# Performance work log

Measured on AMD Instinct MI355X. Metric: run time of the kernel, lower is better.

The kernel has to match this reference:

```python
import jax, jax.numpy as jnp
import numpy as np

D_OUT = 10          # number of classes (d_out)
TEMP = 1.0          # temperature T
EPS = 1e-07         # log eps from original code


def setup_inputs() -> dict:
    key = jax.random.key(0)
    k1, k2, k3, k4, k5 = jax.random.split(key, 5)
    N, M, d_in, dim = 2048, 131072, 128, 128
    x = jax.random.normal(k1, (N, d_in), dtype=jnp.float32)
    candidate_x = jax.random.normal(k2, (M, d_in), dtype=jnp.float32)
    candidate_y = jax.random.randint(k3, (M,), 0, D_OUT)
    # encoder = nn.Linear(d_in, dim): weight [dim, d_in], bias [dim]
    W = jax.random.normal(k4, (dim, d_in), dtype=jnp.float32) / np.float32(np.sqrt(d_in))
    b = jax.random.normal(k5, (dim,), dtype=jnp.float32) * 0.01
    return {"x": x, "candidate_x": candidate_x, "candidate_y": candidate_y, "W": W, "b": b}


def reference(x, candidate_x, candidate_y, W, b):
    # encoder (mode=0, n_blocks=0): single linear layer
    z = x @ W.T + b                 # [N, dim]
    zc = candidate_x @ W.T + b      # [M, dim]
    # torch.cdist(z, zc, p=2): pairwise euclidean distances [N, M]
    sq = (jnp.sum(z * z, axis=-1, keepdims=True)
          + jnp.sum(zc * zc, axis=-1)[None, :]
          - 2.0 * (z @ zc.T))
    dist = jnp.sqrt(jnp.maximum(sq, 1e-12)) / TEMP
    # is_train=False: no diagonal masking, no candidate subsampling
    probs = jax.nn.softmax(-dist, axis=-1)            # [N, M]
    onehot = jax.nn.one_hot(candidate_y, D_OUT, dtype=z.dtype)  # [M, D_OUT]
    logits = probs @ onehot                           # [N, D_OUT]
    return jnp.log(logits + EPS)
```

## Files before the change

kernel.cpp:

```cpp
#include <hip/hip_runtime.h>
#include <stdint.h>
#include <math.h>

#define N_ROWS 2048
#define M_CAND 131072
#define DIMK 128
#define DOUT 10
#define COLS_PER_BLOCK 1024
#define SUB_ITERS 16
#define CHUNKS_MAX 138
#define M_PAD_MAX (CHUNKS_MAX * COLS_PER_BLOCK)
#define LOG2E 1.4426950408889634f
#define L2E2 (LOG2E * LOG2E)

typedef __attribute__((ext_vector_type(8))) __bf16 bf16x8;
typedef __attribute__((ext_vector_type(8))) short s16x8;
typedef __attribute__((ext_vector_type(4))) float f32x4;
typedef __attribute__((address_space(3))) void lds_void;
typedef const __attribute__((address_space(1))) void gbl_void;

__device__ __forceinline__ short f2bf(float f) {
  union { float f; unsigned u; } v; v.f = f;
  return (short)((v.u + 0x7fffu + ((v.u >> 16) & 1u)) >> 16);
}
__device__ __forceinline__ float bf2f(short h) {
  union { unsigned u; float f; } v;
  v.u = ((unsigned)(unsigned short)h) << 16; return v.f;
}
__device__ __forceinline__ float fast_sqrtf(float x) {
#if __has_builtin(__builtin_amdgcn_sqrtf)
  return __builtin_amdgcn_sqrtf(x);
#else
  return sqrtf(x);
#endif
}
__device__ __forceinline__ float fast_exp2f(float x) {
#if __has_builtin(__builtin_amdgcn_exp2f)
  return __builtin_amdgcn_exp2f(x);
#else
  return exp2f(x);
#endif
}

__device__ __forceinline__ void stage64(const short* gbase, short* lds, int t) {
  int w = t >> 6;
#pragma unroll
  for (int i = 0; i < 4; ++i) {
    int flat = i * 256 + t;
    int r = flat >> 4, s = flat & 15;
    int g = s ^ (r & 15);
    const short* src = gbase + r * DIMK + g * 8;
    short* dst = lds + (i * 256 + w * 64) * 8;
    __builtin_amdgcn_global_load_lds((gbl_void*)src, (lds_void*)dst, 16, 0, 0);
  }
}

__device__ __forceinline__ void stage128(const short* gbase, short* lds, int t) {
  int w = t >> 6;
#pragma unroll
  for (int i = 0; i < 8; ++i) {
    int flat = i * 256 + t;
    int r = flat >> 4, s = flat & 15;
    int g = s ^ (r & 15);
    const short* src = gbase + r * DIMK + g * 8;
    short* dst = lds + (i * 256 + w * 64) * 8;
    __builtin_amdgcn_global_load_lds((gbl_void*)src, (lds_void*)dst, 16, 0, 0);
  }
}

__device__ __forceinline__ void mfma_tile(const short* As, const short* Bs,
                                          f32x4 acc[4][4], int wrow, int wcol,
                                          int quad, int l15) {
#pragma unroll
  for (int ks = 0; ks < 4; ++ks) {
    int slot = (ks * 4 + quad) ^ l15;
    bf16x8 a[4], b[4];
#pragma unroll
    for (int i = 0; i < 4; ++i) {
      a[i] = *(const bf16x8*)(As + (wrow + i * 16 + l15) * DIMK + slot * 8);
      b[i] = *(const bf16x8*)(Bs + (wcol + i * 16 + l15) * DIMK + slot * 8);
    }
#pragma unroll
    for (int i = 0; i < 4; ++i)
#pragma unroll
      for (int j = 0; j < 4; ++j)
        acc[i][j] = __builtin_amdgcn_mfma_f32_16x16x32_bf16(a[i], b[j], acc[i][j], 0, 0, 0);
  }
}

__global__ __launch_bounds__(256) void fill_kernel(int* __restrict__ p, int v, int n) {
  int i = blockIdx.x * 256 + threadIdx.x;
  if (i < n) p[i] = v;
}

__global__ __launch_bounds__(256) void hist_kernel(const int* __restrict__ y,
                                                   int* __restrict__ cnt) {
  __shared__ int h[DOUT];
  int t = threadIdx.x;
  if (t < DOUT) h[t] = 0;
  __syncthreads();
  atomicAdd(&h[y[blockIdx.x * 256 + t]], 1);
  __syncthreads();
  if (t < DOUT) cnt[blockIdx.x * DOUT + t] = h[t];
}

__global__ __launch_bounds__(512) void scan_kernel(const int* __restrict__ cnt,
                                                   int* __restrict__ blockoff,
                                                   int* __restrict__ chunk_class) {
  __shared__ int buf[2][512 * DOUT];
  __shared__ int pbnd[DOUT + 1];
  int t = threadIdx.x;
  int v[DOUT];
#pragma unroll
  for (int c = 0; c < DOUT; ++c) { v[c] = cnt[t * DOUT + c]; buf[0][t * DOUT + c] = v[c]; }
  __syncthreads();
  int src = 0;
  for (int off = 1; off < 512; off <<= 1) {
    int x[DOUT];
#pragma unroll
    for (int c = 0; c < DOUT; ++c) {
      x[c] = buf[src][t * DOUT + c];
      if (t >= off) x[c] += buf[src][(t - off) * DOUT + c];
    }
#pragma unroll
    for (int c = 0; c < DOUT; ++c) buf[1 - src][t * DOUT + c] = x[c];
    src ^= 1;
    __syncthreads();
  }
  if (t == 0) {
    int pb = 0;
    pbnd[0] = 0;
    for (int c = 0; c < DOUT; ++c) {
      int tot = buf[src][511 * DOUT + c];
      pb += (tot + COLS_PER_BLOCK - 1) & ~(COLS_PER_BLOCK - 1);
      pbnd[c + 1] = pb;
    }
  }
  __syncthreads();
  if (t < CHUNKS_MAX) {
    int col = t * COLS_PER_BLOCK, c = 0;
#pragma unroll
    for (int k = 1; k < DOUT; ++k) c += (col >= pbnd[k]) ? 1 : 0;
    chunk_class[t] = c;
  }
#pragma unroll
  for (int c = 0; c < DOUT; ++c)
    blockoff[t * DOUT + c] = pbnd[c] + buf[src][t * DOUT + c] - v[c];
}

__global__ __launch_bounds__(256) void scatter_kernel(const int* __restrict__ y,
                                                      const int* __restrict__ blockoff,
                                                      int* __restrict__ invperm) {
  __shared__ int cur[DOUT];
  int t = threadIdx.x;
  if (t < DOUT) cur[t] = blockoff[blockIdx.x * DOUT + t];
  __syncthreads();
  int e = blockIdx.x * 256 + t;
  int p = atomicAdd(&cur[y[e]], 1);
  invperm[p] = e;
}

__global__ __launch_bounds__(256, 2) void encoder_kernel(
    const float* __restrict__ X, const float* __restrict__ W,
    const float* __restrict__ bias, const int* __restrict__ invperm,
    short* __restrict__ Zb, float* __restrict__ Sq) {
  __shared__ __align__(16) short As[DIMK * DIMK];
  __shared__ __align__(16) short Bs[DIMK * DIMK];
  __shared__ float bias_s[DIMK];
  __shared__ float sqacc[DIMK];
  int t = threadIdx.x;
  int rowbase = blockIdx.x * 128;
  if (t < DIMK) { bias_s[t] = bias[t]; sqacc[t] = 0.f; }
#pragma unroll
  for (int i = 0; i < 8; ++i) {
    int flat = i * 256 + t;
    int r = flat >> 4, sl = flat & 15;
    int g = sl ^ (r & 15);
    const float* srcW = W + r * DIMK + g * 8;
    float4 a0 = *(const float4*)srcW;
    float4 a1 = *(const float4*)(srcW + 4);
    s16x8 wv;
    wv[0] = f2bf(a0.x); wv[1] = f2bf(a0.y); wv[2] = f2bf(a0.z); wv[3] = f2bf(a0.w);
    wv[4] = f2bf(a1.x); wv[5] = f2bf(a1.y); wv[6] = f2bf(a1.z); wv[7] = f2bf(a1.w);
    *(s16x8*)(Bs + r * DIMK + sl * 8) = wv;
    int xr = rowbase + r;
    int gxr = invperm ? invperm[xr] : xr;
    const float* srcX = X + (size_t)(gxr < 0 ? 0 : gxr) * DIMK + g * 8;
    float4 b0 = *(const float4*)srcX;
    float4 b1 = *(const float4*)(srcX + 4);
    if (gxr < 0) { b0 = make_float4(0.f, 0.f, 0.f, 0.f); b1 = b0; }
    s16x8 xv;
    xv[0] = f2bf(b0.x); xv[1] = f2bf(b0.y); xv[2] = f2bf(b0.z); xv[3] = f2bf(b0.w);
    xv[4] = f2bf(b1.x); xv[5] = f2bf(b1.y); xv[6] = f2bf(b1.z); xv[7] = f2bf(b1.w);
    *(s16x8*)(As + r * DIMK + sl * 8) = xv;
  }
  __syncthreads();
  int lane = t & 63, wid = t >> 6;
  int quad = lane >> 4, l15 = lane & 15;
  int wrow = (wid >> 1) * 64, wcol = (wid & 1) * 64;
  f32x4 acc[4][4];
  f32x4 z4 = {0.f, 0.f, 0.f, 0.f};
#pragma unroll
  for (int i = 0; i < 4; ++i)
#pragma unroll
    for (int j = 0; j < 4; ++j) acc[i][j] = z4;
  mfma_tile(As, Bs, acc, wrow, wcol, quad, l15);
#pragma unroll
  for (int ti = 0; ti < 4; ++ti) {
#pragma unroll
    for (int r = 0; r < 4; ++r) {
      int row_l = wrow + ti * 16 + quad * 4 + r;
      size_t grow = (size_t)(rowbase + row_l);
      float sqp = 0.f;
#pragma unroll
      for (int j = 0; j < 4; ++j) {
        int dcol = wcol + j * 16 + l15;
        float z = acc[ti][j][r] + bias_s[dcol];
        short hb = f2bf(z);
        float zr = bf2f(hb);
        sqp += zr * zr;
        Zb[grow * DIMK + dcol] = hb;
      }
      sqp += __shfl_xor(sqp, 1);
      sqp += __shfl_xor(sqp, 2);
      sqp += __shfl_xor(sqp, 4);
      sqp += __shfl_xor(sqp, 8);
      if (l15 == 0) atomicAdd(&sqacc[row_l], sqp);
    }
  }
  __syncthreads();
  if (t < DIMK) {
    bool dead = invperm && (invperm[rowbase + t] < 0);
    Sq[rowbase + t] = dead ? 1e30f : sqacc[t];
  }
}

__global__ __launch_bounds__(256, 4) void nca_main(
    const short* __restrict__ Zb, const short* __restrict__ Cb,
    const float* __restrict__ Sqz, const float* __restrict__ Sqc,
    float* __restrict__ partials) {
  __shared__ __align__(16) short Bs[2][64 * DIMK];
  __shared__ float sqc_s[COLS_PER_BLOCK];

  int t = threadIdx.x;
  int lane = t & 63, wid = t >> 6;
  int quad = lane >> 4, l15 = lane & 15;
  int wrow = wid * 32;
  int rowbase = blockIdx.x * 128;
  int colbase0 = blockIdx.y * COLS_PER_BLOCK;

  stage64(Cb + (size_t)colbase0 * DIMK, &Bs[0][0], t);

#pragma unroll
  for (int i = 0; i < 4; ++i)
    sqc_s[i * 256 + t] = Sqc[colbase0 + i * 256 + t] * L2E2;

  bf16x8 afrag[4][2];
#pragma unroll
  for (int ks = 0; ks < 4; ++ks)
#pragma unroll
    for (int ti = 0; ti < 2; ++ti)
      afrag[ks][ti] = *(const bf16x8*)(
          Zb + (size_t)(rowbase + wrow + ti * 16 + l15) * DIMK + ks * 32 + quad * 8);

  float szv[2][4];
#pragma unroll
  for (int ti = 0; ti < 2; ++ti)
#pragma unroll
    for (int r = 0; r < 4; ++r)
      szv[ti][r] = Sqz[rowbase + wrow + ti * 16 + quad * 4 + r] * L2E2;

  float sum[8];
#pragma unroll
  for (int i = 0; i < 8; ++i) sum[i] = 0.f;

  for (int it = 0; it < SUB_ITERS; ++it) {
    __syncthreads();
    if (it + 1 < SUB_ITERS)
      stage64(Cb + (size_t)(colbase0 + (it + 1) * 64) * DIMK, &Bs[(it + 1) & 1][0], t);
    const short* B = &Bs[it & 1][0];

    f32x4 acc[2][4];
    f32x4 z4 = {0.f, 0.f, 0.f, 0.f};
#pragma unroll
    for (int ti = 0; ti < 2; ++ti)
#pragma unroll
      for (int j = 0; j < 4; ++j) acc[ti][j] = z4;

#pragma unroll
    for (int ks = 0; ks < 4; ++ks) {
      int slot = (ks * 4 + quad) ^ l15;
      bf16x8 b[4];
#pragma unroll
      for (int j = 0; j < 4; ++j)
        b[j] = *(const bf16x8*)(B + (j * 16 + l15) * DIMK + slot * 8);
#pragma unroll
      for (int ti = 0; ti < 2; ++ti)
#pragma unroll
        for (int j = 0; j < 4; ++j)
          acc[ti][j] = __builtin_amdgcn_mfma_f32_16x16x32_bf16(afrag[ks][ti], b[j],
                                                               acc[ti][j], 0, 0, 0);
    }

    float sqcv[4];
#pragma unroll
    for (int j = 0; j < 4; ++j) sqcv[j] = sqc_s[it * 64 + j * 16 + l15];
#pragma unroll
    for (int ti = 0; ti < 2; ++ti)
#pragma unroll
      for (int r = 0; r < 4; ++r) {
        float base = szv[ti][r];
        float v[4];
#pragma unroll
        for (int j = 0; j < 4; ++j) {
          float sq = fmaf(acc[ti][j][r], -2.0f * L2E2, base + sqcv[j]);
          float d = fast_sqrtf(__builtin_fabsf(sq));
          v[j] = fast_exp2f(-d);
        }
        sum[ti * 4 + r] += (v[0] + v[1]) + (v[2] + v[3]);
      }
  }

#pragma unroll
  for (int si = 0; si < 8; ++si) {
    float s = sum[si];
    s += __shfl_xor(s, 1);
    s += __shfl_xor(s, 2);
    s += __shfl_xor(s, 4);
    s += __shfl_xor(s, 8);
    if (l15 == 0) {
      int row_l = wrow + (si >> 2) * 16 + quad * 4 + (si & 3);
      partials[(size_t)blockIdx.y * N_ROWS + rowbase + row_l] = s;
    }
  }
}

__global__ __launch_bounds__(64) void reduce_kernel(const float* __restrict__ partials,
                                                    const int* __restrict__ chunk_class,
                                                    float* __restrict__ out) {
  int row = blockIdx.x, lane = threadIdx.x;
  float s = 0.f;
  for (int ch = 0; ch < CHUNKS_MAX; ++ch) {
    float p = partials[(size_t)ch * N_ROWS + row];
    int c = chunk_class[ch];
    s += (lane == c) ? p : 0.f;
  }
  float tot = s;
  tot += __shfl_xor(tot, 1);
  tot += __shfl_xor(tot, 2);
  tot += __shfl_xor(tot, 4);
  tot += __shfl_xor(tot, 8);
  tot += __shfl_xor(tot, 16);
  tot += __shfl_xor(tot, 32);
  if (lane < DOUT)
    out[(size_t)row * DOUT + lane] = logf(s / tot + 1e-7f);
}

extern "C" void kernel_launch(void* const* d_in, const int* in_sizes, int n_in,
                              void* d_out, int out_size, void* d_ws, size_t ws_size,
                              hipStream_t stream) {
  const float* x = (const float*)d_in[0];
  const float* cx = (const float*)d_in[1];
  const int* cy = (const int*)d_in[2];
  const float* W = (const float*)d_in[3];
  const float* bias = (const float*)d_in[4];
  float* out = (float*)d_out;
  char* ws = (char*)d_ws;

  size_t off = 0;
  auto alloc = [&](size_t bytes) {
    void* p = ws + off;
    off = (off + bytes + 255) & ~(size_t)255;
    return p;
  };
  short* Zb = (short*)alloc((size_t)N_ROWS * DIMK * 2);
  short* Cb = (short*)alloc((size_t)M_PAD_MAX * DIMK * 2);
  float* Sqz = (float*)alloc((size_t)N_ROWS * 4);
  float* Sqc = (float*)alloc((size_t)M_PAD_MAX * 4);
  int* invperm = (int*)alloc((size_t)M_PAD_MAX * 4);
  int* cnt = (int*)alloc(512 * DOUT * 4);
  int* blockoff = (int*)alloc(512 * DOUT * 4);
  int* chunk_class = (int*)alloc(CHUNKS_MAX * 4);
  float* partials = (float*)alloc((size_t)CHUNKS_MAX * N_ROWS * 4);
  if (off > ws_size) return;

  fill_kernel<<<(M_PAD_MAX + 255) / 256, 256, 0, stream>>>(invperm, -1, M_PAD_MAX);
  hist_kernel<<<M_CAND / 256, 256, 0, stream>>>(cy, cnt);
  scan_kernel<<<1, 512, 0, stream>>>(cnt, blockoff, chunk_class);
  scatter_kernel<<<M_CAND / 256, 256, 0, stream>>>(cy, blockoff, invperm);
  encoder_kernel<<<N_ROWS / 128, 256, 0, stream>>>(x, W, bias, nullptr, Zb, Sqz);
  encoder_kernel<<<M_PAD_MAX / 128, 256, 0, stream>>>(cx, W, bias, invperm, Cb, Sqc);
  nca_main<<<dim3(N_ROWS / 128, CHUNKS_MAX), 256, 0, stream>>>(Zb, Cb, Sqz, Sqc, partials);
  reduce_kernel<<<N_ROWS, 64, 0, stream>>>(partials, chunk_class, out);
}
```

Before: 262.9 us.

## Remove per-class chunk padding; split mixed-class chunks with masked sums and atomics

```diff
diff --git a/kernel.cpp b/kernel.cpp
--- a/kernel.cpp
+++ b/kernel.cpp
@@ -8,14 +8,14 @@
 #define DOUT 10
 #define COLS_PER_BLOCK 1024
 #define SUB_ITERS 16
-#define CHUNKS_MAX 138
-#define M_PAD_MAX (CHUNKS_MAX * COLS_PER_BLOCK)
+#define CHUNKS (M_CAND / COLS_PER_BLOCK)
 #define LOG2E 1.4426950408889634f
 #define L2E2 (LOG2E * LOG2E)
 
 typedef __attribute__((ext_vector_type(8))) __bf16 bf16x8;
 typedef __attribute__((ext_vector_type(8))) short s16x8;
 typedef __attribute__((ext_vector_type(4))) float f32x4;
+typedef __attribute__((ext_vector_type(2))) float f32x2;
 typedef __attribute__((address_space(3))) void lds_void;
 typedef const __attribute__((address_space(1))) void gbl_void;
 
@@ -55,19 +55,6 @@
   }
 }
 
-__device__ __forceinline__ void stage128(const short* gbase, short* lds, int t) {
-  int w = t >> 6;
-#pragma unroll
-  for (int i = 0; i < 8; ++i) {
-    int flat = i * 256 + t;
-    int r = flat >> 4, s = flat & 15;
-    int g = s ^ (r & 15);
-    const short* src = gbase + r * DIMK + g * 8;
-    short* dst = lds + (i * 256 + w * 64) * 8;
-    __builtin_amdgcn_global_load_lds((gbl_void*)src, (lds_void*)dst, 16, 0, 0);
-  }
-}
-
 __device__ __forceinline__ void mfma_tile(const short* As, const short* Bs,
                                           f32x4 acc[4][4], int wrow, int wcol,
                                           int quad, int l15) {
@@ -88,15 +75,12 @@
   }
 }
 
-__global__ __launch_bounds__(256) void fill_kernel(int* __restrict__ p, int v, int n) {
-  int i = blockIdx.x * 256 + threadIdx.x;
-  if (i < n) p[i] = v;
-}
-
 __global__ __launch_bounds__(256) void hist_kernel(const int* __restrict__ y,
-                                                   int* __restrict__ cnt) {
+                                                   int* __restrict__ cnt,
+                                                   float* __restrict__ accum) {
   __shared__ int h[DOUT];
   int t = threadIdx.x;
+  if (blockIdx.x < 128) accum[blockIdx.x * 256 + t] = 0.f;
   if (t < DOUT) h[t] = 0;
   __syncthreads();
   atomicAdd(&h[y[blockIdx.x * 256 + t]], 1);
@@ -106,9 +90,9 @@
 
 __global__ __launch_bounds__(512) void scan_kernel(const int* __restrict__ cnt,
                                                    int* __restrict__ blockoff,
-                                                   int* __restrict__ chunk_class) {
+                                                   int* __restrict__ bnd_g) {
   __shared__ int buf[2][512 * DOUT];
-  __shared__ int pbnd[DOUT + 1];
+  __shared__ int bnd[DOUT + 1];
   int t = threadIdx.x;
   int v[DOUT];
 #pragma unroll
@@ -128,24 +112,14 @@
     __syncthreads();
   }
   if (t == 0) {
-    int pb = 0;
-    pbnd[0] = 0;
-    for (int c = 0; c < DOUT; ++c) {
-      int tot = buf[src][511 * DOUT + c];
-      pb += (tot + COLS_PER_BLOCK - 1) & ~(COLS_PER_BLOCK - 1);
-      pbnd[c + 1] = pb;
-    }
-  }
-  __syncthreads();
-  if (t < CHUNKS_MAX) {
-    int col = t * COLS_PER_BLOCK, c = 0;
-#pragma unroll
-    for (int k = 1; k < DOUT; ++k) c += (col >= pbnd[k]) ? 1 : 0;
-    chunk_class[t] = c;
-  }
+    bnd[0] = 0;
+    for (int c = 0; c < DOUT; ++c) bnd[c + 1] = bnd[c] + buf[src][511 * DOUT + c];
+    for (int k = 0; k <= DOUT; ++k) bnd_g[k] = bnd[k];
+  }
+  __syncthreads();
 #pragma unroll
   for (int c = 0; c < DOUT; ++c)
-    blockoff[t * DOUT + c] = pbnd[c] + buf[src][t * DOUT + c] - v[c];
+    blockoff[t * DOUT + c] = bnd[c] + buf[src][t * DOUT + c] - v[c];
 }
 
 __global__ __launch_bounds__(256) void scatter_kernel(const int* __restrict__ y,
@@ -185,10 +159,9 @@
     *(s16x8*)(Bs + r * DIMK + sl * 8) = wv;
     int xr = rowbase + r;
     int gxr = invperm ? invperm[xr] : xr;
-    const float* srcX = X + (size_t)(gxr < 0 ? 0 : gxr) * DIMK + g * 8;
+    const float* srcX = X + (size_t)gxr * DIMK + g * 8;
     float4 b0 = *(const float4*)srcX;
     float4 b1 = *(const float4*)(srcX + 4);
-    if (gxr < 0) { b0 = make_float4(0.f, 0.f, 0.f, 0.f); b1 = b0; }
     s16x8 xv;
     xv[0] = f2bf(b0.x); xv[1] = f2bf(b0.y); xv[2] = f2bf(b0.z); xv[3] = f2bf(b0.w);
     xv[4] = f2bf(b1.x); xv[5] = f2bf(b1.y); xv[6] = f2bf(b1.z); xv[7] = f2bf(b1.w);
@@ -229,18 +202,14 @@
     }
   }
   __syncthreads();
-  if (t < DIMK) {
-    bool dead = invperm && (invperm[rowbase + t] < 0);
-    Sq[rowbase + t] = dead ? 1e30f : sqacc[t];
-  }
-}
-
-__global__ __launch_bounds__(256, 4) void nca_main(
+  if (t < DIMK) Sq[rowbase + t] = sqacc[t] * L2E2;
+}
+
+__global__ __launch_bounds__(256, 5) void nca_main(
     const short* __restrict__ Zb, const short* __restrict__ Cb,
     const float* __restrict__ Sqz, const float* __restrict__ Sqc,
-    float* __restrict__ partials) {
+    const int* __restrict__ bnd_g, float* __restrict__ accum) {
   __shared__ __align__(16) short Bs[2][64 * DIMK];
-  __shared__ float sqc_s[COLS_PER_BLOCK];
 
   int t = threadIdx.x;
   int lane = t & 63, wid = t >> 6;
@@ -249,11 +218,19 @@
   int rowbase = blockIdx.x * 128;
   int colbase0 = blockIdx.y * COLS_PER_BLOCK;
 
+  int bnd[DOUT + 1];
+#pragma unroll
+  for (int k = 0; k <= DOUT; ++k) bnd[k] = bnd_g[k];
+  int cls_lo = 0, cls_hi = 0;
+#pragma unroll
+  for (int k = 1; k < DOUT; ++k) {
+    cls_lo += (colbase0 >= bnd[k]) ? 1 : 0;
+    cls_hi += (colbase0 + COLS_PER_BLOCK - 1 >= bnd[k]) ? 1 : 0;
+  }
+  bool two = (cls_hi != cls_lo);
+  int split = bnd[cls_hi];
+
   stage64(Cb + (size_t)colbase0 * DIMK, &Bs[0][0], t);
-
-#pragma unroll
-  for (int i = 0; i < 4; ++i)
-    sqc_s[i * 256 + t] = Sqc[colbase0 + i * 256 + t] * L2E2;
 
   bf16x8 afrag[4][2];
 #pragma unroll
@@ -263,21 +240,30 @@
       afrag[ks][ti] = *(const bf16x8*)(
           Zb + (size_t)(rowbase + wrow + ti * 16 + l15) * DIMK + ks * 32 + quad * 8);
 
-  float szv[2][4];
-#pragma unroll
-  for (int ti = 0; ti < 2; ++ti)
-#pragma unroll
-    for (int r = 0; r < 4; ++r)
-      szv[ti][r] = Sqz[rowbase + wrow + ti * 16 + quad * 4 + r] * L2E2;
-
-  float sum[8];
-#pragma unroll
-  for (int i = 0; i < 8; ++i) sum[i] = 0.f;
+  f32x2 szv2[2][2];
+#pragma unroll
+  for (int ti = 0; ti < 2; ++ti) {
+    f32x4 s4 = *(const f32x4*)(Sqz + rowbase + wrow + ti * 16 + quad * 4);
+    szv2[ti][0] = (f32x2){s4[0], s4[1]};
+    szv2[ti][1] = (f32x2){s4[2], s4[3]};
+  }
+
+  float sum[8], sumB[8];
+#pragma unroll
+  for (int i = 0; i < 8; ++i) { sum[i] = 0.f; sumB[i] = 0.f; }
+
+  const f32x2 m2 = {-2.0f, -2.0f};
 
   for (int it = 0; it < SUB_ITERS; ++it) {
+    int colb = colbase0 + it * 64;
     __syncthreads();
+
+    float sqcv[4];
+#pragma unroll
+    for (int j = 0; j < 4; ++j) sqcv[j] = Sqc[colb + j * 16 + l15];
+
     if (it + 1 < SUB_ITERS)
-      stage64(Cb + (size_t)(colbase0 + (it + 1) * 64) * DIMK, &Bs[(it + 1) & 1][0], t);
+      stage64(Cb + (size_t)(colb + 64) * DIMK, &Bs[(it + 1) & 1][0], t);
     const short* B = &Bs[it & 1][0];
 
     f32x4 acc[2][4];
@@ -290,35 +276,67 @@
 #pragma unroll
     for (int ks = 0; ks < 4; ++ks) {
       int slot = (ks * 4 + quad) ^ l15;
-      bf16x8 b[4];
+      const short* p = B + l15 * DIMK + slot * 8;
+      bf16x8 b0 = *(const bf16x8*)(p);
+      bf16x8 b1 = *(const bf16x8*)(p + 16 * DIMK);
+      bf16x8 b2 = *(const bf16x8*)(p + 32 * DIMK);
+      bf16x8 b3 = *(const bf16x8*)(p + 48 * DIMK);
+#pragma unroll
+      for (int ti = 0; ti < 2; ++ti) {
+        acc[ti][0] = __builtin_amdgcn_mfma_f32_16x16x32_bf16(afrag[ks][ti], b0, acc[ti][0], 0, 0, 0);
+        acc[ti][1] = __builtin_amdgcn_mfma_f32_16x16x32_bf16(afrag[ks][ti], b1, acc[ti][1], 0, 0, 0);
+        acc[ti][2] = __builtin_amdgcn_mfma_f32_16x16x32_bf16(afrag[ks][ti], b2, acc[ti][2], 0, 0, 0);
+        acc[ti][3] = __builtin_amdgcn_mfma_f32_16x16x32_bf16(afrag[ks][ti], b3, acc[ti][3], 0, 0, 0);
+      }
+    }
+
+    if (!two) {
+#pragma unroll
+      for (int ti = 0; ti < 2; ++ti)
+#pragma unroll
+        for (int j = 0; j < 4; ++j) {
+          f32x2 q = {sqcv[j], sqcv[j]};
+          f32x2 s01 = szv2[ti][0] + q;
+          f32x2 s23 = szv2[ti][1] + q;
+          f32x4 a = acc[ti][j];
+          f32x2 a01 = {a[0], a[1]}, a23 = {a[2], a[3]};
+          s01 = a01 * m2 + s01;
+          s23 = a23 * m2 + s23;
+          float e0 = fast_exp2f(-fast_sqrtf(__builtin_fabsf(s01[0])));
+          float e1 = fast_exp2f(-fast_sqrtf(__builtin_fabsf(s01[1])));
+          float e2 = fast_exp2f(-fast_sqrtf(__builtin_fabsf(s23[0])));
+          float e3 = fast_exp2f(-fast_sqrtf(__builtin_fabsf(s23[1])));
+          sum[ti * 4 + 0] += e0; sum[ti * 4 + 1] += e1;
+          sum[ti * 4 + 2] += e2; sum[ti * 4 + 3] += e3;
+        }
+    } else {
+      float mask[4];
 #pragma unroll
       for (int j = 0; j < 4; ++j)
-        b[j] = *(const bf16x8*)(B + (j * 16 + l15) * DIMK + slot * 8);
+        mask[j] = (colb + j * 16 + l15 >= split) ? 1.0f : 0.0f;
 #pragma unroll
       for (int ti = 0; ti < 2; ++ti)
 #pragma unroll
-        for (int j = 0; j < 4; ++j)
-          acc[ti][j] = __builtin_amdgcn_mfma_f32_16x16x32_bf16(afrag[ks][ti], b[j],
-                                                               acc[ti][j], 0, 0, 0);
-    }
-
-    float sqcv[4];
-#pragma unroll
-    for (int j = 0; j < 4; ++j) sqcv[j] = sqc_s[it * 64 + j * 16 + l15];
-#pragma unroll
-    for (int ti = 0; ti < 2; ++ti)
-#pragma unroll
-      for (int r = 0; r < 4; ++r) {
-        float base = szv[ti][r];
-        float v[4];
-#pragma unroll
         for (int j = 0; j < 4; ++j) {
-          float sq = fmaf(acc[ti][j][r], -2.0f * L2E2, base + sqcv[j]);
-          float d = fast_sqrtf(__builtin_fabsf(sq));
-          v[j] = fast_exp2f(-d);
+          f32x2 q = {sqcv[j], sqcv[j]};
+          f32x2 s01 = szv2[ti][0] + q;
+          f32x2 s23 = szv2[ti][1] + q;
+          f32x4 a = acc[ti][j];
+          f32x2 a01 = {a[0], a[1]}, a23 = {a[2], a[3]};
+          s01 = a01 * m2 + s01;
+          s23 = a23 * m2 + s23;
+          float e0 = fast_exp2f(-fast_sqrtf(__builtin_fabsf(s01[0])));
+          float e1 = fast_exp2f(-fast_sqrtf(__builtin_fabsf(s01[1])));
+          float e2 = fast_exp2f(-fast_sqrtf(__builtin_fabsf(s23[0])));
+          float e3 = fast_exp2f(-fast_sqrtf(__builtin_fabsf(s23[1])));
+          sum[ti * 4 + 0] += e0; sum[ti * 4 + 1] += e1;
+          sum[ti * 4 + 2] += e2; sum[ti * 4 + 3] += e3;
+          sumB[ti * 4 + 0] = fmaf(e0, mask[j], sumB[ti * 4 + 0]);
+          sumB[ti * 4 + 1] = fmaf(e1, mask[j], sumB[ti * 4 + 1]);
+          sumB[ti * 4 + 2] = fmaf(e2, mask[j], sumB[ti * 4 + 2]);
+          sumB[ti * 4 + 3] = fmaf(e3, mask[j], sumB[ti * 4 + 3]);
         }
-        sum[ti * 4 + r] += (v[0] + v[1]) + (v[2] + v[3]);
-      }
+    }
   }
 
 #pragma unroll
@@ -328,32 +346,36 @@
     s += __shfl_xor(s, 2);
     s += __shfl_xor(s, 4);
     s += __shfl_xor(s, 8);
+    float b = sumB[si];
+    if (two) {
+      b += __shfl_xor(b, 1);
+      b += __shfl_xor(b, 2);
+      b += __shfl_xor(b, 4);
+      b += __shfl_xor(b, 8);
+    }
     if (l15 == 0) {
-      int row_l = wrow + (si >> 2) * 16 + quad * 4 + (si & 3);
-      partials[(size_t)blockIdx.y * N_ROWS + rowbase + row_l] = s;
-    }
-  }
-}
-
-__global__ __launch_bounds__(64) void reduce_kernel(const float* __restrict__ partials,
-                                                    const int* __restrict__ chunk_class,
-                                                    float* __restrict__ out) {
-  int row = blockIdx.x, lane = threadIdx.x;
-  float s = 0.f;
-  for (int ch = 0; ch < CHUNKS_MAX; ++ch) {
-    float p = partials[(size_t)ch * N_ROWS + row];
-    int c = chunk_class[ch];
-    s += (lane == c) ? p : 0.f;
-  }
-  float tot = s;
-  tot += __shfl_xor(tot, 1);
-  tot += __shfl_xor(tot, 2);
-  tot += __shfl_xor(tot, 4);
-  tot += __shfl_xor(tot, 8);
-  tot += __shfl_xor(tot, 16);
-  tot += __shfl_xor(tot, 32);
-  if (lane < DOUT)
-    out[(size_t)row * DOUT + lane] = logf(s / tot + 1e-7f);
+      int row = rowbase + wrow + (si >> 2) * 16 + quad * 4 + (si & 3);
+      if (!two) {
+        atomicAdd(&accum[row * 16 + cls_lo], s);
+      } else {
+        atomicAdd(&accum[row * 16 + cls_lo], s - b);
+        atomicAdd(&accum[row * 16 + cls_hi], b);
+      }
+    }
+  }
+}
+
+__global__ __launch_bounds__(256) void logits_kernel(const float* __restrict__ accum,
+                                                     float* __restrict__ out) {
+  int i = blockIdx.x * 256 + threadIdx.x;
+  if (i >= N_ROWS) return;
+  float v[DOUT], tot = 0.f;
+#pragma unroll
+  for (int c = 0; c < DOUT; ++c) { v[c] = accum[i * 16 + c]; tot += v[c]; }
+  float inv = 1.0f / tot;
+#pragma unroll
+  for (int c = 0; c < DOUT; ++c)
+    out[(size_t)i * DOUT + c] = logf(fmaf(v[c], inv, 1e-7f));
 }
 
 extern "C" void kernel_launch(void* const* d_in, const int* in_sizes, int n_in,
@@ -374,22 +396,21 @@
     return p;
   };
   short* Zb = (short*)alloc((size_t)N_ROWS * DIMK * 2);
-  short* Cb = (short*)alloc((size_t)M_PAD_MAX * DIMK * 2);
+  short* Cb = (short*)alloc((size_t)M_CAND * DIMK * 2);
   float* Sqz = (float*)alloc((size_t)N_ROWS * 4);
-  float* Sqc = (float*)alloc((size_t)M_PAD_MAX * 4);
-  int* invperm = (int*)alloc((size_t)M_PAD_MAX * 4);
+  float* Sqc = (float*)alloc((size_t)M_CAND * 4);
+  int* invperm = (int*)alloc((size_t)M_CAND * 4);
   int* cnt = (int*)alloc(512 * DOUT * 4);
   int* blockoff = (int*)alloc(512 * DOUT * 4);
-  int* chunk_class = (int*)alloc(CHUNKS_MAX * 4);
-  float* partials = (float*)alloc((size_t)CHUNKS_MAX * N_ROWS * 4);
+  int* bnd = (int*)alloc((DOUT + 1) * 4);
+  float* accum = (float*)alloc((size_t)N_ROWS * 16 * 4);
   if (off > ws_size) return;
 
-  fill_kernel<<<(M_PAD_MAX + 255) / 256, 256, 0, stream>>>(invperm, -1, M_PAD_MAX);
-  hist_kernel<<<M_CAND / 256, 256, 0, stream>>>(cy, cnt);
-  scan_kernel<<<1, 512, 0, stream>>>(cnt, blockoff, chunk_class);
+  hist_kernel<<<M_CAND / 256, 256, 0, stream>>>(cy, cnt, accum);
+  scan_kernel<<<1, 512, 0, stream>>>(cnt, blockoff, bnd);
   scatter_kernel<<<M_CAND / 256, 256, 0, stream>>>(cy, blockoff, invperm);
   encoder_kernel<<<N_ROWS / 128, 256, 0, stream>>>(x, W, bias, nullptr, Zb, Sqz);
-  encoder_kernel<<<M_PAD_MAX / 128, 256, 0, stream>>>(cx, W, bias, invperm, Cb, Sqc);
-  nca_main<<<dim3(N_ROWS / 128, CHUNKS_MAX), 256, 0, stream>>>(Zb, Cb, Sqz, Sqc, partials);
-  reduce_kernel<<<N_ROWS, 64, 0, stream>>>(partials, chunk_class, out);
-}
+  encoder_kernel<<<M_CAND / 128, 256, 0, stream>>>(cx, W, bias, invperm, Cb, Sqc);
+  nca_main<<<dim3(N_ROWS / 128, CHUNKS), 256, 0, stream>>>(Zb, Cb, Sqz, Sqc, bnd, accum);
+  logits_kernel<<<(N_ROWS + 255) / 256, 256, 0, stream>>>(accum, out);
+}
```

After: 420.7 us. 60.0% more time.
